# Kernel optimization log

Measured on AMD Instinct MI355X. Metric: run time of the kernel, lower is better.

## Reference

```python
import jax, jax.numpy as jnp
import numpy as np

N, E = 100000, 1600000
IN_C, HID, OUT = 128, 64, 25
EPS = 1e-5


def gcn_conv(x, row, col, W, b):
    # PyG GCNConv: h = x@W; add self-loops; sym-norm D^-1/2 A D^-1/2; + bias
    h = x @ W                                   # [N, F]
    ones = jnp.ones(row.shape[0], h.dtype)
    deg = jax.ops.segment_sum(ones, col, num_segments=N) + 1.0  # +1 self-loop
    dinv = jax.lax.rsqrt(deg)                   # [N]
    norm = dinv[row] * dinv[col]                # [E]
    agg = jax.ops.segment_sum(h[row] * norm[:, None], col, num_segments=N)
    agg = agg + (dinv * dinv)[:, None] * h      # self-loop contribution
    return agg + b


def layer_norm(x, w, b):
    # PyG LayerNorm mode='node': normalize each node over feature dim
    mu = jnp.mean(x, axis=-1, keepdims=True)
    var = jnp.var(x, axis=-1, keepdims=True)
    return (x - mu) * jax.lax.rsqrt(var + EPS) * w + b


def setup_inputs() -> dict:
    key = jax.random.key(0)
    ks = jax.random.split(key, 16)
    x = jax.random.normal(ks[0], (N, IN_C), dtype=jnp.float32)
    edge_index = jax.random.randint(ks[1], (2, E), 0, N, dtype=jnp.int32)

    def glorot(k, shp):
        lim = float(np.sqrt(6.0 / (shp[0] + shp[1])))
        return jax.random.uniform(k, shp, jnp.float32, -lim, lim)

    return {
        "x": x,
        "edge_index": edge_index,
        "W1": glorot(ks[2], (IN_C, HID)), "b1": jnp.zeros((HID,), jnp.float32),
        "W2": glorot(ks[3], (HID, HID)), "b2": jnp.zeros((HID,), jnp.float32),
        "W3": glorot(ks[4], (HID, HID)), "b3": jnp.zeros((HID,), jnp.float32),
        "ln1_w": jnp.ones((HID,), jnp.float32), "ln1_b": jnp.zeros((HID,), jnp.float32),
        "ln2_w": jnp.ones((HID,), jnp.float32), "ln2_b": jnp.zeros((HID,), jnp.float32),
        "ln3_w": jnp.ones((HID,), jnp.float32), "ln3_b": jnp.zeros((HID,), jnp.float32),
        "Wl": glorot(ks[5], (HID, OUT)), "bl": jnp.zeros((OUT,), jnp.float32),
    }


def reference(x, edge_index, W1, b1, W2, b2, W3, b3,
              ln1_w, ln1_b, ln2_w, ln2_b, ln3_w, ln3_b, Wl, bl):
    row, col = edge_index[0], edge_index[1]
    h = jax.nn.relu(layer_norm(gcn_conv(x, row, col, W1, b1), ln1_w, ln1_b))
    h = jax.nn.relu(layer_norm(gcn_conv(h, row, col, W2, b2), ln2_w, ln2_b))
    h = jax.nn.relu(layer_norm(gcn_conv(h, row, col, W3, b3), ln3_w, ln3_b))
    pooled = jnp.mean(h, axis=0)                # [HID]
    return pooled @ Wl + bl                     # [OUT]
```

## Files before the change

### kernel.cpp

```cpp
#include <hip/hip_runtime.h>
#include <hip/hip_bf16.h>

typedef __hip_bfloat16 bf16;
typedef __attribute__((ext_vector_type(8))) short short8;
typedef __attribute__((ext_vector_type(4))) float f32x4;
typedef __attribute__((ext_vector_type(2))) float f32x2;

#define HID 64
#define CAP 4096
#define BSH 7
#define EPB 4096
#define SMAX 2048

__device__ __forceinline__ float bfbits2f(unsigned short b){
    union { unsigned u; float f; } c; c.u = ((unsigned)b) << 16; return c.f;
}
__device__ __forceinline__ unsigned short f2bfbits(float x){
    union { float f; unsigned u; } c; c.f = x;
    unsigned r = c.u + 0x7fffu + ((c.u >> 16) & 1u);
    return (unsigned short)(r >> 16);
}
__device__ __forceinline__ unsigned char f2fp8(float x){
    unsigned v = __builtin_amdgcn_cvt_pk_fp8_f32(x, x, 0u, false);
    return (unsigned char)(v & 0xffu);
}
template<bool HI>
__device__ __forceinline__ f32x2 cvtpk(unsigned u){
    return __builtin_amdgcn_cvt_pk_f32_fp8(u, HI);
}


__global__ __launch_bounds__(1024) void bin_kernel(const int* __restrict__ row,
                                                   const int* __restrict__ col,
                                                   int E, int NB,
                                                   int* __restrict__ gCur,
                                                   int* __restrict__ binned){
    __shared__ int lCnt[1024];
    __shared__ int lOff[1024];
    __shared__ int lGB[1024];
    __shared__ int sPay[EPB];
    __shared__ unsigned short sB[EPB];
    __shared__ int wSum[16];
    int tid = threadIdx.x;
    int lane = tid & 63, wv = tid >> 6;
    int e0 = blockIdx.x * EPB;
    int eN = E - e0; if (eN > EPB) eN = EPB;

    lCnt[tid] = 0;
    int cols[4], rows[4];
    #pragma unroll
    for (int k = 0; k < 4; ++k){
        int i = tid + k * 1024;
        bool ok = (i < eN);
        cols[k] = ok ? col[e0 + i] : -1;
        rows[k] = ok ? row[e0 + i] : 0;
    }
    __syncthreads();
    #pragma unroll
    for (int k = 0; k < 4; ++k)
        if (cols[k] >= 0) atomicAdd(&lCnt[cols[k] >> BSH], 1);
    __syncthreads();

    int c = lCnt[tid];
    int inc = c;
    #pragma unroll
    for (int m = 1; m < 64; m <<= 1){
        int t = __shfl_up(inc, m);
        if (lane >= m) inc += t;
    }
    if (lane == 63) wSum[wv] = inc;
    __syncthreads();
    if (wv == 0 && lane < 16){
        int orig = wSum[lane];
        int ws = orig;
        #pragma unroll
        for (int m = 1; m < 16; m <<= 1){
            int t = __shfl_up(ws, m);
            if (lane >= m) ws += t;
        }
        wSum[lane] = ws - orig;
    }
    __syncthreads();
    int excl = inc - c + wSum[wv];
    lOff[tid] = excl;
    if (c){
        int gb = atomicAdd(&gCur[tid], c);
        lGB[tid] = tid * CAP + gb - excl;
    }
    lCnt[tid] = 0;
    __syncthreads();

    #pragma unroll
    for (int k = 0; k < 4; ++k){
        if (cols[k] >= 0){
            int bk = cols[k] >> BSH;
            int rk = atomicAdd(&lCnt[bk], 1);
            int pos = lOff[bk] + rk;
            sPay[pos] = ((cols[k] & 127) << 17) | rows[k];
            sB[pos] = (unsigned short)bk;
        }
    }
    __syncthreads();

    #pragma unroll
    for (int k = 0; k < 4; ++k){
        int i = tid + k * 1024;
        if (i < eN){
            int bk = sB[i];
            int tgt = lGB[bk] + i;
            if (tgt - (bk << 12) < CAP)
                binned[tgt] = sPay[i];
        }
    }
}


__global__ __launch_bounds__(512) void build_kernel(const int* __restrict__ gCur,
                                                    const int* __restrict__ binned,
                                                    int* __restrict__ csr_row,
                                                    int* __restrict__ col_ptr,
                                                    int* __restrict__ col_end,
                                                    float* __restrict__ dinv, int N){
    __shared__ int sBin[CAP];
    __shared__ int sCsr[CAP];
    __shared__ int fineCnt[128];
    __shared__ int sc[128];
    __shared__ int fineCur[128];
    int b = blockIdx.x, tid = threadIdx.x;
    int j0 = b * CAP;
    int cnt = gCur[b];
    if (cnt > CAP) cnt = CAP;
    for (int i = tid; i < cnt; i += 512) sBin[i] = binned[j0 + i];
    if (tid < 128) fineCnt[tid] = 0;
    __syncthreads();
    for (int i = tid; i < cnt; i += 512)
        atomicAdd(&fineCnt[sBin[i] >> 17], 1);
    __syncthreads();
    if (tid < 128){
        int lane = tid & 63, w = tid >> 6;
        int cf = fineCnt[tid];
        int inc = cf;
        #pragma unroll
        for (int m = 1; m < 64; m <<= 1){
            int t = __shfl_up(inc, m);
            if (lane >= m) inc += t;
        }
        if (lane == 63) sc[w] = inc;
        __syncthreads();
        int waveOff = (w == 1) ? sc[0] : 0;
        int startL = waveOff + inc - cf;
        fineCur[tid] = startL;
        int node = (b << BSH) + tid;
        if (node < N){
            col_ptr[node] = j0 + startL;
            col_end[node] = j0 + startL + cf;
            dinv[node] = rsqrtf((float)cf + 1.0f);
        }
    } else {
        __syncthreads();
    }
    __syncthreads();
    for (int i = tid; i < cnt; i += 512){
        int w = sBin[i];
        int pos = atomicAdd(&fineCur[w >> 17], 1);
        sCsr[pos] = w & 0x1FFFF;
    }
    __syncthreads();
    for (int i = tid; i < cnt; i += 512) csr_row[j0 + i] = sCsr[i];
}


template<int K, typename T>
__global__ __launch_bounds__(256) void matmul_kernel(const T* __restrict__ act,
                                                     const float* __restrict__ W,
                                                     const float* __restrict__ dinv,
                                                     unsigned char* __restrict__ H8, int N){
    constexpr int KS = K / 32;
    constexpr int RB = 2 * K;
    __shared__ __align__(16) short As[128 * K];
    __shared__ __align__(16) short Wt[64 * K];

    int tid = threadIdx.x;
    int nodeBase = blockIdx.x * 128;

    for (int i = tid; i < K * 64; i += 256){
        int k = i >> 6, c = i & 63;
        unsigned short b = f2bfbits(W[i]);
        int byte = c * RB + ((2 * k) ^ ((c & 7) << 4));
        *(short*)((char*)Wt + byte) = (short)b;
    }
    constexpr int OPR = K / 8;
    for (int i = tid; i < 128 * OPR; i += 256){
        int node = i / OPR, oct = i % OPR;
        int n = nodeBase + node;
        short8 v = (short8)0;
        if (n < N){
            if constexpr (sizeof(T) == 4){
                const float4* xp = (const float4*)&act[(size_t)n * K + oct * 8];
                float4 a = xp[0], b = xp[1];
                v[0] = (short)f2bfbits(a.x); v[1] = (short)f2bfbits(a.y);
                v[2] = (short)f2bfbits(a.z); v[3] = (short)f2bfbits(a.w);
                v[4] = (short)f2bfbits(b.x); v[5] = (short)f2bfbits(b.y);
                v[6] = (short)f2bfbits(b.z); v[7] = (short)f2bfbits(b.w);
            } else {
                v = *(const short8*)&act[(size_t)n * K + oct * 8];
            }
        }
        int byte = node * RB + ((oct * 16) ^ ((node & 7) << 4));
        *(short8*)((char*)As + byte) = v;
    }
    __syncthreads();

    int wv = tid >> 6, l = tid & 63;
    int lr = l & 15, lg = l >> 4;

    short8 bfr[KS][4];
    #pragma unroll
    for (int ks = 0; ks < KS; ++ks)
        #pragma unroll
        for (int t = 0; t < 4; ++t){
            int c = t * 16 + lr;
            int byte = c * RB + ((ks * 64 + lg * 16) ^ ((c & 7) << 4));
            bfr[ks][t] = *(const short8*)((const char*)Wt + byte);
        }

    #pragma unroll
    for (int nt = 0; nt < 2; ++nt){
        int nb = wv * 32 + nt * 16;
        int node = nb + lr;
        short8 af[KS];
        #pragma unroll
        for (int ks = 0; ks < KS; ++ks){
            int byte = node * RB + ((ks * 64 + lg * 16) ^ ((node & 7) << 4));
            af[ks] = *(const short8*)((const char*)As + byte);
        }
        f32x4 acc[4] = {(f32x4)0.f, (f32x4)0.f, (f32x4)0.f, (f32x4)0.f};
        #pragma unroll
        for (int ks = 0; ks < KS; ++ks)
            #pragma unroll
            for (int t = 0; t < 4; ++t)
                acc[t] = __builtin_amdgcn_mfma_f32_16x16x32_bf16(af[ks], bfr[ks][t], acc[t], 0, 0, 0);
        #pragma unroll
        for (int r = 0; r < 4; ++r){
            int n = nodeBase + nb + lg * 4 + r;
            if (n < N){
                float dv = dinv[n];
                #pragma unroll
                for (int t = 0; t < 4; ++t)
                    H8[((size_t)(unsigned)n << 6) + t * 16 + lr] = f2fp8(acc[t][r] * dv);
            }
        }
    }
}


template<bool POOL>
__global__ __launch_bounds__(256) void agg_ln_kernel(const unsigned char* __restrict__ H8,
                                                     const float* __restrict__ dinv,
                                                     const int* __restrict__ col_ptr,
                                                     const int* __restrict__ col_end,
                                                     const int* __restrict__ csr_row,
                                                     const float* __restrict__ bias,
                                                     const float* __restrict__ lnw,
                                                     const float* __restrict__ lnb,
                                                     bf16* __restrict__ out,
                                                     float* __restrict__ pooledRep, int N){
    __shared__ int sIdx[2 * SMAX];
    __shared__ float sp[4][64];
    int tid = threadIdx.x;
    int wid = tid >> 6, l = tid & 63;
    int g = l >> 3, s = l & 7;
    int nodeBase = blockIdx.x * 32;
    int n = nodeBase + wid * 8 + g;
    bool valid = (n < N);
    int nc = valid ? n : nodeBase;

    int lastN = nodeBase + 31; if (lastN > N - 1) lastN = N - 1;
    int jlo = col_ptr[nodeBase];
    int jhi = col_end[lastN];
    int cnt = jhi - jlo;

    int j0 = col_ptr[nc];
    int j1 = valid ? col_end[nc] : j0;
    int deg = j1 - j0;

    bool fast = (cnt <= SMAX);
    if (fast){
        for (int i = tid; i < cnt; i += 256) sIdx[i] = csr_row[jlo + i];
    }
    __syncthreads();

    unsigned soff = (unsigned)(s << 3);
    const char* Hb = (const char*)H8;
    uint2 us = *(const uint2*)(Hb + ((((unsigned)nc) << 6) | soff));

    int mdeg = deg;
    mdeg = max(mdeg, __shfl_xor(mdeg, 8));
    mdeg = max(mdeg, __shfl_xor(mdeg, 16));
    mdeg = max(mdeg, __shfl_xor(mdeg, 32));

    f32x2 a0 = {0.f,0.f}, a1 = {0.f,0.f}, a2 = {0.f,0.f}, a3 = {0.f,0.f};

#define ACC(u)  { a0 += cvtpk<false>((u).x); a1 += cvtpk<true>((u).x); \
                  a2 += cvtpk<false>((u).y); a3 += cvtpk<true>((u).y); }
#define GLOOP(IDX) \
    for (int i = 0; i < mdeg; i += 4){ \
        int r0 = (i     < deg) ? IDX(i    ) : N; \
        int r1 = (i + 1 < deg) ? IDX(i + 1) : N; \
        int r2 = (i + 2 < deg) ? IDX(i + 2) : N; \
        int r3 = (i + 3 < deg) ? IDX(i + 3) : N; \
        uint2 u0 = *(const uint2*)(Hb + ((((unsigned)r0) << 6) | soff)); \
        uint2 u1 = *(const uint2*)(Hb + ((((unsigned)r1) << 6) | soff)); \
        uint2 u2 = *(const uint2*)(Hb + ((((unsigned)r2) << 6) | soff)); \
        uint2 u3 = *(const uint2*)(Hb + ((((unsigned)r3) << 6) | soff)); \
        ACC(u0) ACC(u1) ACC(u2) ACC(u3) \
    }

    if (fast){
        int p = j0 - jlo;
#define IDXF(e) sIdx[p + (e)]
        GLOOP(IDXF)
#undef IDXF
    } else {
#define IDXS(e) csr_row[j0 + (e)]
        GLOOP(IDXS)
#undef IDXS
    }
#undef GLOOP
#undef ACC

    a0 += cvtpk<false>(us.x); a1 += cvtpk<true>(us.x);
    a2 += cvtpk<false>(us.y); a3 += cvtpk<true>(us.y);

    float dv = dinv[nc];
    float4 b4a = ((const float4*)bias)[2 * s];
    float4 b4b = ((const float4*)bias)[2 * s + 1];
    float v0 = fmaf(dv, a0.x, b4a.x), v1 = fmaf(dv, a0.y, b4a.y);
    float v2 = fmaf(dv, a1.x, b4a.z), v3 = fmaf(dv, a1.y, b4a.w);
    float v4 = fmaf(dv, a2.x, b4b.x), v5 = fmaf(dv, a2.y, b4b.y);
    float v6 = fmaf(dv, a3.x, b4b.z), v7 = fmaf(dv, a3.y, b4b.w);

    float sum = ((v0 + v1) + (v2 + v3)) + ((v4 + v5) + (v6 + v7));
    #pragma unroll
    for (int m = 1; m < 8; m <<= 1) sum += __shfl_xor(sum, m);
    float mu = sum * (1.0f / 64.0f);
    float d0 = v0 - mu, d1 = v1 - mu, d2 = v2 - mu, d3 = v3 - mu;
    float d4 = v4 - mu, d5 = v5 - mu, d6 = v6 - mu, d7 = v7 - mu;
    float var = ((d0*d0 + d1*d1) + (d2*d2 + d3*d3)) + ((d4*d4 + d5*d5) + (d6*d6 + d7*d7));
    #pragma unroll
    for (int m = 1; m < 8; m <<= 1) var += __shfl_xor(var, m);
    float rstd = rsqrtf(var * (1.0f / 64.0f) + 1e-5f);
    float4 w4a = ((const float4*)lnw)[2 * s];
    float4 w4b = ((const float4*)lnw)[2 * s + 1];
    float4 c4a = ((const float4*)lnb)[2 * s];
    float4 c4b = ((const float4*)lnb)[2 * s + 1];
    float y0 = fmaxf(fmaf(d0 * rstd, w4a.x, c4a.x), 0.0f);
    float y1 = fmaxf(fmaf(d1 * rstd, w4a.y, c4a.y), 0.0f);
    float y2 = fmaxf(fmaf(d2 * rstd, w4a.z, c4a.z), 0.0f);
    float y3 = fmaxf(fmaf(d3 * rstd, w4a.w, c4a.w), 0.0f);
    float y4 = fmaxf(fmaf(d4 * rstd, w4b.x, c4b.x), 0.0f);
    float y5 = fmaxf(fmaf(d5 * rstd, w4b.y, c4b.y), 0.0f);
    float y6 = fmaxf(fmaf(d6 * rstd, w4b.z, c4b.z), 0.0f);
    float y7 = fmaxf(fmaf(d7 * rstd, w4b.w, c4b.w), 0.0f);

    if (POOL){
        float z0 = valid ? y0 : 0.f, z1 = valid ? y1 : 0.f;
        float z2 = valid ? y2 : 0.f, z3 = valid ? y3 : 0.f;
        float z4 = valid ? y4 : 0.f, z5 = valid ? y5 : 0.f;
        float z6 = valid ? y6 : 0.f, z7 = valid ? y7 : 0.f;
        #pragma unroll
        for (int m = 8; m < 64; m <<= 1){
            z0 += __shfl_xor(z0, m); z1 += __shfl_xor(z1, m);
            z2 += __shfl_xor(z2, m); z3 += __shfl_xor(z3, m);
            z4 += __shfl_xor(z4, m); z5 += __shfl_xor(z5, m);
            z6 += __shfl_xor(z6, m); z7 += __shfl_xor(z7, m);
        }
        if (g == 0){
            ((float4*)sp[wid])[2 * s]     = make_float4(z0, z1, z2, z3);
            ((float4*)sp[wid])[2 * s + 1] = make_float4(z4, z5, z6, z7);
        }
        __syncthreads();
        if (tid < 64){
            float t = sp[0][tid] + sp[1][tid] + sp[2][tid] + sp[3][tid];
            atomicAdd(&pooledRep[(blockIdx.x & 63) * 64 + tid], t);
        }
    } else {
        if (valid){
            short8 o;
            o[0] = (short)f2bfbits(y0); o[1] = (short)f2bfbits(y1);
            o[2] = (short)f2bfbits(y2); o[3] = (short)f2bfbits(y3);
            o[4] = (short)f2bfbits(y4); o[5] = (short)f2bfbits(y5);
            o[6] = (short)f2bfbits(y6); o[7] = (short)f2bfbits(y7);
            *(short8*)((short*)out + (((size_t)(unsigned)nc) << 6) + (s << 3)) = o;
        }
    }
}


__global__ __launch_bounds__(64) void final_kernel(const float* __restrict__ pooledRep,
                                                   const float* __restrict__ Wl,
                                                   const float* __restrict__ bl,
                                                   float* __restrict__ outp, float invN){
    __shared__ float pooled[64];
    int t = threadIdx.x;
    float s = 0.f;
    #pragma unroll 8
    for (int r = 0; r < 64; ++r) s += pooledRep[r * 64 + t];
    pooled[t] = s;
    __syncthreads();
    if (t < 25){
        float acc = bl[t];
        #pragma unroll 8
        for (int f = 0; f < HID; ++f)
            acc = fmaf(pooled[f] * invN, Wl[f * 25 + t], acc);
        outp[t] = acc;
    }
}


static inline size_t alignup(size_t x){ return (x + 255) & ~(size_t)255; }

extern "C" void kernel_launch(void* const* d_in, const int* in_sizes, int n_in,
                              void* d_out, int out_size, void* d_ws, size_t ws_size,
                              hipStream_t stream) {
    const float* x   = (const float*)d_in[0];
    const int*   ei  = (const int*)d_in[1];
    const float* W1  = (const float*)d_in[2];
    const float* b1  = (const float*)d_in[3];
    const float* W2  = (const float*)d_in[4];
    const float* b2  = (const float*)d_in[5];
    const float* W3  = (const float*)d_in[6];
    const float* b3  = (const float*)d_in[7];
    const float* ln1w = (const float*)d_in[8];
    const float* ln1b = (const float*)d_in[9];
    const float* ln2w = (const float*)d_in[10];
    const float* ln2b = (const float*)d_in[11];
    const float* ln3w = (const float*)d_in[12];
    const float* ln3b = (const float*)d_in[13];
    const float* Wl  = (const float*)d_in[14];
    const float* bl  = (const float*)d_in[15];

    const int N = in_sizes[0] / 128;
    const int E = in_sizes[1] / 2;
    const int NB = (N + 127) >> BSH;
    const int* row = ei;
    const int* col = ei + E;

    char* p = (char*)d_ws;
    int*   gCur      = (int*)p;   p += alignup((size_t)NB * 4);
    float* pooledRep = (float*)p; p += alignup(64 * 64 * 4);
    size_t zeroBytes = (size_t)((char*)p - (char*)gCur);
    int*   binned    = (int*)p;   p += alignup((size_t)NB * CAP * 4);
    int*   csr_row   = (int*)p;   p += alignup((size_t)NB * CAP * 4);
    int*   col_ptr   = (int*)p;   p += alignup((size_t)N * 4);
    int*   col_end   = (int*)p;   p += alignup((size_t)N * 4);
    float* dinv      = (float*)p; p += alignup((size_t)N * 4);
    unsigned char* H8 = (unsigned char*)p; p += alignup(((size_t)N + 1) * HID);
    bf16*  A         = (bf16*)p;  p += alignup((size_t)N * HID * 2);

    hipMemsetAsync(gCur, 0, zeroBytes, stream);
    hipMemsetAsync(H8 + (size_t)N * HID, 0, HID, stream);

    int gB = (E + EPB - 1) / EPB;
    int gM = (N + 127) / 128;
    int gA = (N + 31) / 32;

    bin_kernel<<<gB, 1024, 0, stream>>>(row, col, E, NB, gCur, binned);
    build_kernel<<<NB, 512, 0, stream>>>(gCur, binned, csr_row, col_ptr, col_end, dinv, N);

    matmul_kernel<128, float><<<gM, 256, 0, stream>>>(x, W1, dinv, H8, N);
    agg_ln_kernel<false><<<gA, 256, 0, stream>>>(H8, dinv, col_ptr, col_end, csr_row,
                                                 b1, ln1w, ln1b, A, pooledRep, N);
    matmul_kernel<64, bf16><<<gM, 256, 0, stream>>>(A, W2, dinv, H8, N);
    agg_ln_kernel<false><<<gA, 256, 0, stream>>>(H8, dinv, col_ptr, col_end, csr_row,
                                                 b2, ln2w, ln2b, A, pooledRep, N);
    matmul_kernel<64, bf16><<<gM, 256, 0, stream>>>(A, W3, dinv, H8, N);
    agg_ln_kernel<true><<<gA, 256, 0, stream>>>(H8, dinv, col_ptr, col_end, csr_row,
                                                b3, ln3w, ln3b, A, pooledRep, N);

    final_kernel<<<1, 64, 0, stream>>>(pooledRep, Wl, bl, (float*)d_out, 1.0f / (float)N);
}
```

Measured before the change: 245.8 us.

## Fuse next-layer matmul into aggregation+LayerNorm kernel with double-buffered FP8 features

The next layer's linear transform (bf16 MFMA with a swizzled LDS copy of W) now runs inside the aggregation/LayerNorm kernel, so the separate layer-2 and layer-3 matmul kernels and the bf16 intermediate write and read go away. Each block now handles 64 nodes with 4 lanes per node and 16-byte gathers instead of 8-byte ones. FP8 feature buffers ping-pong between two arrays, and their zero sentinel rows are now cleared inside build_kernel instead of by a memset. In exchange every agg block converts W to bf16 into LDS, uses more registers and shared memory, and may run at lower occupancy.

New measurement: 241.2 us. No clear change (-1.9%).

```diff
diff --git a/kernel.cpp b/kernel.cpp
--- a/kernel.cpp
+++ b/kernel.cpp
@@ -120,13 +120,20 @@
                                                     int* __restrict__ csr_row,
                                                     int* __restrict__ col_ptr,
                                                     int* __restrict__ col_end,
-                                                    float* __restrict__ dinv, int N){
+                                                    float* __restrict__ dinv,
+                                                    unsigned char* __restrict__ H8a,
+                                                    unsigned char* __restrict__ H8b, int N){
     __shared__ int sBin[CAP];
     __shared__ int sCsr[CAP];
     __shared__ int fineCnt[128];
     __shared__ int sc[128];
     __shared__ int fineCur[128];
     int b = blockIdx.x, tid = threadIdx.x;
+    if (b == 0 && tid >= 480){
+        int t = tid - 480;
+        if (t < 16) ((unsigned*)(H8a + ((size_t)N << 6)))[t] = 0u;
+        else        ((unsigned*)(H8b + ((size_t)N << 6)))[t - 16] = 0u;
+    }
     int j0 = b * CAP;
     int cnt = gCur[b];
     if (cnt > CAP) cnt = CAP;
@@ -255,27 +262,30 @@
 
 
 template<bool POOL>
-__global__ __launch_bounds__(256) void agg_ln_kernel(const unsigned char* __restrict__ H8,
-                                                     const float* __restrict__ dinv,
-                                                     const int* __restrict__ col_ptr,
-                                                     const int* __restrict__ col_end,
-                                                     const int* __restrict__ csr_row,
-                                                     const float* __restrict__ bias,
-                                                     const float* __restrict__ lnw,
-                                                     const float* __restrict__ lnb,
-                                                     bf16* __restrict__ out,
-                                                     float* __restrict__ pooledRep, int N){
+__global__ __launch_bounds__(256) void agg_kernel(const unsigned char* __restrict__ H8in,
+                                                  const float* __restrict__ dinv,
+                                                  const int* __restrict__ col_ptr,
+                                                  const int* __restrict__ col_end,
+                                                  const int* __restrict__ csr_row,
+                                                  const float* __restrict__ bias,
+                                                  const float* __restrict__ lnw,
+                                                  const float* __restrict__ lnb,
+                                                  const float* __restrict__ Wn,
+                                                  unsigned char* __restrict__ H8out,
+                                                  float* __restrict__ pooledRep, int N){
     __shared__ int sIdx[2 * SMAX];
-    __shared__ float sp[4][64];
+    __shared__ __align__(16) short ybuf[POOL ? 8 : 4096];
+    __shared__ __align__(16) short Wt[POOL ? 8 : 4096];
+    __shared__ float sp[POOL ? 256 : 4];
     int tid = threadIdx.x;
     int wid = tid >> 6, l = tid & 63;
-    int g = l >> 3, s = l & 7;
-    int nodeBase = blockIdx.x * 32;
-    int n = nodeBase + wid * 8 + g;
+    int g = l >> 2, s = l & 3;
+    int nodeBase = blockIdx.x * 64;
+    int n = nodeBase + wid * 16 + g;
     bool valid = (n < N);
     int nc = valid ? n : nodeBase;
 
-    int lastN = nodeBase + 31; if (lastN > N - 1) lastN = N - 1;
+    int lastN = nodeBase + 63; if (lastN > N - 1) lastN = N - 1;
     int jlo = col_ptr[nodeBase];
     int jhi = col_end[lastN];
     int cnt = jhi - jlo;
@@ -288,32 +298,44 @@
     if (fast){
         for (int i = tid; i < cnt; i += 256) sIdx[i] = csr_row[jlo + i];
     }
-    __syncthreads();
-
-    unsigned soff = (unsigned)(s << 3);
-    const char* Hb = (const char*)H8;
-    uint2 us = *(const uint2*)(Hb + ((((unsigned)nc) << 6) | soff));
+    if (!POOL){
+        for (int i = tid; i < 4096; i += 256){
+            int k = i >> 6, c = i & 63;
+            unsigned short b = f2bfbits(Wn[i]);
+            int byte = c * 128 + ((2 * k) ^ ((c & 7) << 4));
+            *(short*)((char*)Wt + byte) = (short)b;
+        }
+    }
+    __syncthreads();
+
+    unsigned soff = (unsigned)(s << 4);
+    const char* Hb = (const char*)H8in;
+    uint4 us = *(const uint4*)(Hb + ((((unsigned)nc) << 6) | soff));
 
     int mdeg = deg;
+    mdeg = max(mdeg, __shfl_xor(mdeg, 4));
     mdeg = max(mdeg, __shfl_xor(mdeg, 8));
     mdeg = max(mdeg, __shfl_xor(mdeg, 16));
     mdeg = max(mdeg, __shfl_xor(mdeg, 32));
 
     f32x2 a0 = {0.f,0.f}, a1 = {0.f,0.f}, a2 = {0.f,0.f}, a3 = {0.f,0.f};
-
-#define ACC(u)  { a0 += cvtpk<false>((u).x); a1 += cvtpk<true>((u).x); \
-                  a2 += cvtpk<false>((u).y); a3 += cvtpk<true>((u).y); }
+    f32x2 a4 = {0.f,0.f}, a5 = {0.f,0.f}, a6 = {0.f,0.f}, a7 = {0.f,0.f};
+
+#define ACC4(u) { a0 += cvtpk<false>((u).x); a1 += cvtpk<true>((u).x); \
+                  a2 += cvtpk<false>((u).y); a3 += cvtpk<true>((u).y); \
+                  a4 += cvtpk<false>((u).z); a5 += cvtpk<true>((u).z); \
+                  a6 += cvtpk<false>((u).w); a7 += cvtpk<true>((u).w); }
 #define GLOOP(IDX) \
     for (int i = 0; i < mdeg; i += 4){ \
         int r0 = (i     < deg) ? IDX(i    ) : N; \
         int r1 = (i + 1 < deg) ? IDX(i + 1) : N; \
         int r2 = (i + 2 < deg) ? IDX(i + 2) : N; \
         int r3 = (i + 3 < deg) ? IDX(i + 3) : N; \
-        uint2 u0 = *(const uint2*)(Hb + ((((unsigned)r0) << 6) | soff)); \
-        uint2 u1 = *(const uint2*)(Hb + ((((unsigned)r1) << 6) | soff)); \
-        uint2 u2 = *(const uint2*)(Hb + ((((unsigned)r2) << 6) | soff)); \
-        uint2 u3 = *(const uint2*)(Hb + ((((unsigned)r3) << 6) | soff)); \
-        ACC(u0) ACC(u1) ACC(u2) ACC(u3) \
+        uint4 u0 = *(const uint4*)(Hb + ((((unsigned)r0) << 6) | soff)); \
+        uint4 u1 = *(const uint4*)(Hb + ((((unsigned)r1) << 6) | soff)); \
+        uint4 u2 = *(const uint4*)(Hb + ((((unsigned)r2) << 6) | soff)); \
+        uint4 u3 = *(const uint4*)(Hb + ((((unsigned)r3) << 6) | soff)); \
+        ACC4(u0) ACC4(u1) ACC4(u2) ACC4(u3) \
     }
 
     if (fast){
@@ -327,71 +349,106 @@
 #undef IDXS
     }
 #undef GLOOP
-#undef ACC
-
+#undef ACC4
+
+    ACC_SELF: ;
     a0 += cvtpk<false>(us.x); a1 += cvtpk<true>(us.x);
     a2 += cvtpk<false>(us.y); a3 += cvtpk<true>(us.y);
+    a4 += cvtpk<false>(us.z); a5 += cvtpk<true>(us.z);
+    a6 += cvtpk<false>(us.w); a7 += cvtpk<true>(us.w);
 
     float dv = dinv[nc];
-    float4 b4a = ((const float4*)bias)[2 * s];
-    float4 b4b = ((const float4*)bias)[2 * s + 1];
-    float v0 = fmaf(dv, a0.x, b4a.x), v1 = fmaf(dv, a0.y, b4a.y);
-    float v2 = fmaf(dv, a1.x, b4a.z), v3 = fmaf(dv, a1.y, b4a.w);
-    float v4 = fmaf(dv, a2.x, b4b.x), v5 = fmaf(dv, a2.y, b4b.y);
-    float v6 = fmaf(dv, a3.x, b4b.z), v7 = fmaf(dv, a3.y, b4b.w);
-
-    float sum = ((v0 + v1) + (v2 + v3)) + ((v4 + v5) + (v6 + v7));
-    #pragma unroll
-    for (int m = 1; m < 8; m <<= 1) sum += __shfl_xor(sum, m);
+    float acc16[16] = { a0.x, a0.y, a1.x, a1.y, a2.x, a2.y, a3.x, a3.y,
+                        a4.x, a4.y, a5.x, a5.y, a6.x, a6.y, a7.x, a7.y };
+    float v[16], y[16];
+    float4 bq[4], wq[4], cq[4];
+    #pragma unroll
+    for (int q = 0; q < 4; ++q){
+        bq[q] = ((const float4*)bias)[(s << 2) + q];
+        wq[q] = ((const float4*)lnw)[(s << 2) + q];
+        cq[q] = ((const float4*)lnb)[(s << 2) + q];
+    }
+    #pragma unroll
+    for (int j = 0; j < 16; ++j)
+        v[j] = fmaf(dv, acc16[j], ((const float*)&bq[j >> 2])[j & 3]);
+
+    float sum = 0.f;
+    #pragma unroll
+    for (int j = 0; j < 16; ++j) sum += v[j];
+    sum += __shfl_xor(sum, 1); sum += __shfl_xor(sum, 2);
     float mu = sum * (1.0f / 64.0f);
-    float d0 = v0 - mu, d1 = v1 - mu, d2 = v2 - mu, d3 = v3 - mu;
-    float d4 = v4 - mu, d5 = v5 - mu, d6 = v6 - mu, d7 = v7 - mu;
-    float var = ((d0*d0 + d1*d1) + (d2*d2 + d3*d3)) + ((d4*d4 + d5*d5) + (d6*d6 + d7*d7));
-    #pragma unroll
-    for (int m = 1; m < 8; m <<= 1) var += __shfl_xor(var, m);
+    float var = 0.f;
+    #pragma unroll
+    for (int j = 0; j < 16; ++j){ float d = v[j] - mu; var = fmaf(d, d, var); }
+    var += __shfl_xor(var, 1); var += __shfl_xor(var, 2);
     float rstd = rsqrtf(var * (1.0f / 64.0f) + 1e-5f);
-    float4 w4a = ((const float4*)lnw)[2 * s];
-    float4 w4b = ((const float4*)lnw)[2 * s + 1];
-    float4 c4a = ((const float4*)lnb)[2 * s];
-    float4 c4b = ((const float4*)lnb)[2 * s + 1];
-    float y0 = fmaxf(fmaf(d0 * rstd, w4a.x, c4a.x), 0.0f);
-    float y1 = fmaxf(fmaf(d1 * rstd, w4a.y, c4a.y), 0.0f);
-    float y2 = fmaxf(fmaf(d2 * rstd, w4a.z, c4a.z), 0.0f);
-    float y3 = fmaxf(fmaf(d3 * rstd, w4a.w, c4a.w), 0.0f);
-    float y4 = fmaxf(fmaf(d4 * rstd, w4b.x, c4b.x), 0.0f);
-    float y5 = fmaxf(fmaf(d5 * rstd, w4b.y, c4b.y), 0.0f);
-    float y6 = fmaxf(fmaf(d6 * rstd, w4b.z, c4b.z), 0.0f);
-    float y7 = fmaxf(fmaf(d7 * rstd, w4b.w, c4b.w), 0.0f);
+    #pragma unroll
+    for (int j = 0; j < 16; ++j){
+        float d = (v[j] - mu) * rstd;
+        y[j] = fmaxf(fmaf(d, ((const float*)&wq[j >> 2])[j & 3],
+                             ((const float*)&cq[j >> 2])[j & 3]), 0.0f);
+    }
 
     if (POOL){
-        float z0 = valid ? y0 : 0.f, z1 = valid ? y1 : 0.f;
-        float z2 = valid ? y2 : 0.f, z3 = valid ? y3 : 0.f;
-        float z4 = valid ? y4 : 0.f, z5 = valid ? y5 : 0.f;
-        float z6 = valid ? y6 : 0.f, z7 = valid ? y7 : 0.f;
-        #pragma unroll
-        for (int m = 8; m < 64; m <<= 1){
-            z0 += __shfl_xor(z0, m); z1 += __shfl_xor(z1, m);
-            z2 += __shfl_xor(z2, m); z3 += __shfl_xor(z3, m);
-            z4 += __shfl_xor(z4, m); z5 += __shfl_xor(z5, m);
-            z6 += __shfl_xor(z6, m); z7 += __shfl_xor(z7, m);
-        }
-        if (g == 0){
-            ((float4*)sp[wid])[2 * s]     = make_float4(z0, z1, z2, z3);
-            ((float4*)sp[wid])[2 * s + 1] = make_float4(z4, z5, z6, z7);
+        #pragma unroll
+        for (int j = 0; j < 16; ++j){
+            float z = valid ? y[j] : 0.f;
+            z += __shfl_xor(z, 4); z += __shfl_xor(z, 8);
+            z += __shfl_xor(z, 16); z += __shfl_xor(z, 32);
+            y[j] = z;
+        }
+        if (l < 4){
+            #pragma unroll
+            for (int q = 0; q < 4; ++q)
+                ((float4*)sp)[wid * 16 + (s << 2) + q] =
+                    make_float4(y[4*q], y[4*q+1], y[4*q+2], y[4*q+3]);
         }
         __syncthreads();
         if (tid < 64){
-            float t = sp[0][tid] + sp[1][tid] + sp[2][tid] + sp[3][tid];
+            float t = sp[tid] + sp[64 + tid] + sp[128 + tid] + sp[192 + tid];
             atomicAdd(&pooledRep[(blockIdx.x & 63) * 64 + tid], t);
         }
     } else {
-        if (valid){
-            short8 o;
-            o[0] = (short)f2bfbits(y0); o[1] = (short)f2bfbits(y1);
-            o[2] = (short)f2bfbits(y2); o[3] = (short)f2bfbits(y3);
-            o[4] = (short)f2bfbits(y4); o[5] = (short)f2bfbits(y5);
-            o[6] = (short)f2bfbits(y6); o[7] = (short)f2bfbits(y7);
-            *(short8*)((short*)out + (((size_t)(unsigned)nc) << 6) + (s << 3)) = o;
+        char* yb = (char*)ybuf;
+        int base = (wid << 11) + (g << 7);
+        int sw = (g & 7) << 4;
+        short8 ya, yz;
+        #pragma unroll
+        for (int j = 0; j < 8; ++j){ ya[j] = (short)f2bfbits(y[j]); yz[j] = (short)f2bfbits(y[8 + j]); }
+        *(short8*)(yb + base + (((s << 5)     ) ^ sw)) = ya;
+        *(short8*)(yb + base + (((s << 5) + 16) ^ sw)) = yz;
+
+        int lr = l & 15, lg = l >> 4;
+        short8 bfr[2][4];
+        #pragma unroll
+        for (int ks = 0; ks < 2; ++ks)
+            #pragma unroll
+            for (int t = 0; t < 4; ++t){
+                int c = t * 16 + lr;
+                int byte = c * 128 + ((((ks << 2) + lg) << 4) ^ ((c & 7) << 4));
+                bfr[ks][t] = *(const short8*)((const char*)Wt + byte);
+            }
+        short8 af[2];
+        #pragma unroll
+        for (int ks = 0; ks < 2; ++ks){
+            int byte = (wid << 11) + lr * 128 + ((((ks << 2) + lg) << 4) ^ ((lr & 7) << 4));
+            af[ks] = *(const short8*)(yb + byte);
+        }
+        f32x4 acc[4] = {(f32x4)0.f, (f32x4)0.f, (f32x4)0.f, (f32x4)0.f};
+        #pragma unroll
+        for (int ks = 0; ks < 2; ++ks)
+            #pragma unroll
+            for (int t = 0; t < 4; ++t)
+                acc[t] = __builtin_amdgcn_mfma_f32_16x16x32_bf16(af[ks], bfr[ks][t], acc[t], 0, 0, 0);
+        #pragma unroll
+        for (int r = 0; r < 4; ++r){
+            int nn = nodeBase + (wid << 4) + (lg << 2) + r;
+            if (nn < N){
+                float dv2 = dinv[nn];
+                #pragma unroll
+                for (int t = 0; t < 4; ++t)
+                    H8out[((size_t)(unsigned)nn << 6) + t * 16 + lr] = f2fp8(acc[t][r] * dv2);
+            }
         }
     }
 }
@@ -455,28 +512,26 @@
     int*   col_ptr   = (int*)p;   p += alignup((size_t)N * 4);
     int*   col_end   = (int*)p;   p += alignup((size_t)N * 4);
     float* dinv      = (float*)p; p += alignup((size_t)N * 4);
-    unsigned char* H8 = (unsigned char*)p; p += alignup(((size_t)N + 1) * HID);
-    bf16*  A         = (bf16*)p;  p += alignup((size_t)N * HID * 2);
+    unsigned char* H8a = (unsigned char*)p; p += alignup(((size_t)N + 1) * HID);
+    unsigned char* H8b = (unsigned char*)p; p += alignup(((size_t)N + 1) * HID);
 
     hipMemsetAsync(gCur, 0, zeroBytes, stream);
-    hipMemsetAsync(H8 + (size_t)N * HID, 0, HID, stream);
 
     int gB = (E + EPB - 1) / EPB;
     int gM = (N + 127) / 128;
-    int gA = (N + 31) / 32;
+    int gA = (N + 63) / 64;
 
     bin_kernel<<<gB, 1024, 0, stream>>>(row, col, E, NB, gCur, binned);
-    build_kernel<<<NB, 512, 0, stream>>>(gCur, binned, csr_row, col_ptr, col_end, dinv, N);
-
-    matmul_kernel<128, float><<<gM, 256, 0, stream>>>(x, W1, dinv, H8, N);
-    agg_ln_kernel<false><<<gA, 256, 0, stream>>>(H8, dinv, col_ptr, col_end, csr_row,
-                                                 b1, ln1w, ln1b, A, pooledRep, N);
-    matmul_kernel<64, bf16><<<gM, 256, 0, stream>>>(A, W2, dinv, H8, N);
-    agg_ln_kernel<false><<<gA, 256, 0, stream>>>(H8, dinv, col_ptr, col_end, csr_row,
-                                                 b2, ln2w, ln2b, A, pooledRep, N);
-    matmul_kernel<64, bf16><<<gM, 256, 0, stream>>>(A, W3, dinv, H8, N);
-    agg_ln_kernel<true><<<gA, 256, 0, stream>>>(H8, dinv, col_ptr, col_end, csr_row,
-                                                b3, ln3w, ln3b, A, pooledRep, N);
+    build_kernel<<<NB, 512, 0, stream>>>(gCur, binned, csr_row, col_ptr, col_end, dinv,
+                                         H8a, H8b, N);
+
+    matmul_kernel<128, float><<<gM, 256, 0, stream>>>(x, W1, dinv, H8a, N);
+    agg_kernel<false><<<gA, 256, 0, stream>>>(H8a, dinv, col_ptr, col_end, csr_row,
+                                              b1, ln1w, ln1b, W2, H8b, pooledRep, N);
+    agg_kernel<false><<<gA, 256, 0, stream>>>(H8b, dinv, col_ptr, col_end, csr_row,
+                                              b2, ln2w, ln2b, W3, H8a, pooledRep, N);
+    agg_kernel<true><<<gA, 256, 0, stream>>>(H8a, dinv, col_ptr, col_end, csr_row,
+                                             b3, ln3w, ln3b, nullptr, nullptr, pooledRep, N);
 
     final_kernel<<<1, 64, 0, stream>>>(pooledRep, Wl, bl, (float*)d_out, 1.0f / (float)N);
 }
```
